# Kernel optimization log

Measured on AMD Instinct MI355X. Metric: run time of the kernel, lower is better.

Reference implementation:

```python
import jax, jax.numpy as jnp
import numpy as np

N = 50000        # nodes
E = 800000       # edges
IN, H1, H2 = 512, 256, 128
NEG_SLOPE = 0.2


def setup_inputs() -> dict:
    key = jax.random.key(0)
    k = jax.random.split(key, 6)
    X = jax.random.normal(k[0], (N, IN), jnp.float32)
    edge_index = jax.random.randint(k[1], (2, E), 0, N, dtype=jnp.int64)
    # GCNConv params: linear weight (no bias in lin) + additive bias
    W1 = jax.random.normal(k[2], (IN, H1), jnp.float32) / np.sqrt(IN).astype(np.float32)
    b1 = jnp.zeros((H1,), jnp.float32)
    W2 = jax.random.normal(k[3], (H1, H2), jnp.float32) / np.sqrt(H1).astype(np.float32)
    b2 = jnp.zeros((H2,), jnp.float32)
    return {"X": X, "edge_index": edge_index, "W1": W1, "b1": b1, "W2": W2, "b2": b2}


def gcn_conv(x, edge_index, W, b):
    """PyG GCNConv: X' = D^{-1/2} (A + I) D^{-1/2} (X W) + b."""
    src, dst = edge_index[0], edge_index[1]
    # degree with self-loops (unit edge weights)
    deg = jnp.zeros((N,), x.dtype).at[dst].add(jnp.asarray(1.0, x.dtype)) + 1.0
    dinv = jax.lax.rsqrt(deg)
    h = x @ W                                   # dense transform first (in >= out)
    coef = dinv[src] * dinv[dst]                # [E]
    msgs = h[src] * coef[:, None]               # [E, out]
    agg = jax.ops.segment_sum(msgs, dst, num_segments=N)
    agg = agg + (dinv * dinv)[:, None] * h      # self-loop contribution
    return agg + b


def reference(X, edge_index, W1, b1, W2, b2):
    Z = jax.nn.leaky_relu(gcn_conv(X, edge_index, W1, b1), NEG_SLOPE)
    Z = jax.nn.leaky_relu(gcn_conv(Z, edge_index, W2, b2), NEG_SLOPE)
    return Z
```

## Files before the change

kernel.cpp:

```cpp
#include <hip/hip_runtime.h>

constexpr int N_NODES = 50000;
constexpr int N_EDGES = 800000;
constexpr int F_IN  = 512;
constexpr int F_H1  = 256;
constexpr int F_H2  = 128;

typedef short  short8  __attribute__((ext_vector_type(8)));
typedef float  f32x4   __attribute__((ext_vector_type(4)));
typedef unsigned short us4 __attribute__((ext_vector_type(4)));

__device__ __forceinline__ unsigned short bf16_rn(float f) {
  unsigned int u = __float_as_uint(f);
  return (unsigned short)((u + 0x7FFFu + ((u >> 16) & 1u)) >> 16);
}
__device__ __forceinline__ float bf16_tof(unsigned short h) {
  return __uint_as_float(((unsigned int)h) << 16);
}


__global__ __launch_bounds__(256) void k_count(const int* __restrict__ dst,
                                               int* __restrict__ cnt, int e) {
  int i = blockIdx.x * 256 + threadIdx.x;
  if (i < e) atomicAdd(&cnt[dst[i]], 1);
}

__global__ __launch_bounds__(1024) void k_scan(const int* __restrict__ cnt,
                                               int* __restrict__ rowstart,
                                               int* __restrict__ cursor,
                                               float* __restrict__ dinv, int n) {
  __shared__ int wsum[16];
  __shared__ int carry_s;
  const int t = threadIdx.x;
  const int wid = t >> 6, lane = t & 63;
  if (t == 0) { carry_s = 0; rowstart[0] = 0; }
  __syncthreads();
  for (int base = 0; base < n; base += 4096) {
    const int i0 = base + t * 4;
    int v[4];
    if (i0 + 4 <= n) {
      const int4 v4 = *(const int4*)&cnt[i0];
      v[0] = v4.x; v[1] = v4.y; v[2] = v4.z; v[3] = v4.w;
    } else {
#pragma unroll
      for (int j = 0; j < 4; ++j) v[j] = (i0 + j < n) ? cnt[i0 + j] : 0;
    }
#pragma unroll
    for (int j = 0; j < 4; ++j)
      if (i0 + j < n) dinv[i0 + j] = rsqrtf((float)v[j] + 1.0f);
    const int tsum = v[0] + v[1] + v[2] + v[3];
    int x = tsum;
#pragma unroll
    for (int off = 1; off < 64; off <<= 1) {
      int y = __shfl_up(x, off);
      if (lane >= off) x += y;
    }
    if (lane == 63) wsum[wid] = x;
    __syncthreads();
    if (wid == 0) {
      int s = (lane < 16) ? wsum[lane] : 0;
#pragma unroll
      for (int off = 1; off < 16; off <<= 1) {
        int y = __shfl_up(s, off);
        if (lane >= off) s += y;
      }
      if (lane < 16) wsum[lane] = s;
    }
    __syncthreads();
    const int carry = carry_s;
    const int woff = (wid == 0) ? 0 : wsum[wid - 1];
    int run = carry + woff + x - tsum;
#pragma unroll
    for (int j = 0; j < 4; ++j) {
      if (i0 + j < n) {
        cursor[i0 + j] = run;
        run += v[j];
        rowstart[i0 + j + 1] = run;
      }
    }
    __syncthreads();
    if (t == 1023) carry_s = carry + woff + x;
    __syncthreads();
  }
}

__global__ __launch_bounds__(256) void k_fill(const int* __restrict__ src,
                                              const int* __restrict__ dst,
                                              int* __restrict__ cursor,
                                              const float* __restrict__ dinv,
                                              int2* __restrict__ csr, int e) {
  int i = blockIdx.x * 256 + threadIdx.x;
  if (i < e) {
    const int s = src[i], d = dst[i];
    int slot = atomicAdd(&cursor[d], 1);
    csr[slot] = make_int2(s, __float_as_int(dinv[s] * dinv[d]));
  }
}

__global__ __launch_bounds__(256) void k_wsplit2(const float* __restrict__ W1,
                                                 unsigned short* __restrict__ W1h,
                                                 unsigned short* __restrict__ W1l,
                                                 const float* __restrict__ W2,
                                                 unsigned short* __restrict__ W2h,
                                                 unsigned short* __restrict__ W2l) {
  constexpr int T1 = F_IN * F_H1;
  constexpr int T2 = F_H1 * F_H2;
  int id = blockIdx.x * 256 + threadIdx.x;
  if (id < T1) {
    int n = id / F_IN, k = id - n * F_IN;
    float f = W1[(size_t)k * F_H1 + n];
    unsigned short h = bf16_rn(f);
    W1h[id] = h;
    W1l[id] = bf16_rn(f - bf16_tof(h));
  } else if (id < T1 + T2) {
    int id2 = id - T1;
    int n = id2 / F_H1, k = id2 - n * F_H1;
    float f = W2[(size_t)k * F_H2 + n];
    unsigned short h = bf16_rn(f);
    W2h[id2] = h;
    W2l[id2] = bf16_rn(f - bf16_tof(h));
  }
}

template <bool A_IS_F32>
__global__ __launch_bounds__(512, 4) void k_mm(const float* __restrict__ Af,
                                               const unsigned short* __restrict__ Ah,
                                               const unsigned short* __restrict__ Al,
                                               const unsigned short* __restrict__ Bth,
                                               const unsigned short* __restrict__ Btl,
                                               unsigned short* __restrict__ Chh,
                                               unsigned short* __restrict__ Cll,
                                               int M, int N, int K) {
  __shared__ unsigned short Ah_s[128 * 64];
  __shared__ unsigned short Al_s[128 * 64];
  __shared__ unsigned short Bh_s[128 * 64];
  __shared__ unsigned short Bl_s[128 * 64];
  const int tid = threadIdx.x;
  const int wid = tid >> 6, lane = tid & 63;
  const int wm = wid >> 2, wn = wid & 3;
  const int lr = lane & 15, lg = lane >> 4;
  const int row0 = blockIdx.x * 128, col0 = blockIdx.y * 128;

  f32x4 acc[4][2] = {};

  float4 af0[2], af1[2];
  short8 ahr[2], alr[2];
  short8 bhr[2], blr[2];

  const int r_base = tid >> 3, g_ld = tid & 7;

  auto load_tile = [&](int k0) {
#pragma unroll
    for (int c = 0; c < 2; ++c) {
      const int r = c * 64 + r_base;
      const int gr = row0 + r;
      if (A_IS_F32) {
        af0[c] = make_float4(0.f, 0.f, 0.f, 0.f);
        af1[c] = af0[c];
        if (gr < M) {
          const float* ap = Af + (size_t)gr * K + k0 + g_ld * 8;
          af0[c] = *(const float4*)ap;
          af1[c] = *(const float4*)(ap + 4);
        }
      } else {
        ahr[c] = short8{};
        alr[c] = short8{};
        if (gr < M) {
          ahr[c] = *(const short8*)&Ah[(size_t)gr * K + k0 + g_ld * 8];
          alr[c] = *(const short8*)&Al[(size_t)gr * K + k0 + g_ld * 8];
        }
      }
      const int gcol = col0 + r;
      bhr[c] = *(const short8*)&Bth[(size_t)gcol * K + k0 + g_ld * 8];
      blr[c] = *(const short8*)&Btl[(size_t)gcol * K + k0 + g_ld * 8];
    }
  };

  auto store_tile = [&]() {
#pragma unroll
    for (int c = 0; c < 2; ++c) {
      const int r = c * 64 + r_base;
      const int gs = g_ld ^ (r & 7);
      const int doff = r * 64 + gs * 8;
      if (A_IS_F32) {
        const float fv[8] = {af0[c].x, af0[c].y, af0[c].z, af0[c].w,
                             af1[c].x, af1[c].y, af1[c].z, af1[c].w};
        unsigned short hv[8], lv[8];
#pragma unroll
        for (int j = 0; j < 8; ++j) {
          hv[j] = bf16_rn(fv[j]);
          lv[j] = bf16_rn(fv[j] - bf16_tof(hv[j]));
        }
        us4* dh = (us4*)&Ah_s[doff];
        us4* dl = (us4*)&Al_s[doff];
        dh[0] = us4{hv[0], hv[1], hv[2], hv[3]};
        dh[1] = us4{hv[4], hv[5], hv[6], hv[7]};
        dl[0] = us4{lv[0], lv[1], lv[2], lv[3]};
        dl[1] = us4{lv[4], lv[5], lv[6], lv[7]};
      } else {
        *(short8*)&Ah_s[doff] = ahr[c];
        *(short8*)&Al_s[doff] = alr[c];
      }
      *(short8*)&Bh_s[doff] = bhr[c];
      *(short8*)&Bl_s[doff] = blr[c];
    }
  };

  const int nsteps = K >> 6;
  load_tile(0);
  for (int s = 0; s < nsteps; ++s) {
    store_tile();
    __syncthreads();
    if (s + 1 < nsteps) load_tile((s + 1) << 6);
#pragma unroll
    for (int kk = 0; kk < 2; ++kk) {
      short8 ah[4], al[4], bh[2], bl[2];
#pragma unroll
      for (int m = 0; m < 4; ++m) {
        const int r = wm * 64 + m * 16 + lr;
        const int g = kk * 4 + lg;
        const int off = r * 64 + (g ^ (r & 7)) * 8;
        ah[m] = *(const short8*)&Ah_s[off];
        al[m] = *(const short8*)&Al_s[off];
      }
#pragma unroll
      for (int n = 0; n < 2; ++n) {
        const int r = wn * 32 + n * 16 + lr;
        const int g = kk * 4 + lg;
        const int off = r * 64 + (g ^ (r & 7)) * 8;
        bh[n] = *(const short8*)&Bh_s[off];
        bl[n] = *(const short8*)&Bl_s[off];
      }
#pragma unroll
      for (int m = 0; m < 4; ++m)
#pragma unroll
        for (int n = 0; n < 2; ++n)
          acc[m][n] = __builtin_amdgcn_mfma_f32_16x16x32_bf16(ah[m], bh[n],
                                                              acc[m][n], 0, 0, 0);
#pragma unroll
      for (int m = 0; m < 4; ++m)
#pragma unroll
        for (int n = 0; n < 2; ++n) {
          acc[m][n] = __builtin_amdgcn_mfma_f32_16x16x32_bf16(ah[m], bl[n],
                                                              acc[m][n], 0, 0, 0);
          acc[m][n] = __builtin_amdgcn_mfma_f32_16x16x32_bf16(al[m], bh[n],
                                                              acc[m][n], 0, 0, 0);
        }
    }
    __syncthreads();
  }
#pragma unroll
  for (int m = 0; m < 4; ++m) {
#pragma unroll
    for (int j = 0; j < 4; ++j) {
      const int row = row0 + wm * 64 + m * 16 + (lane >> 4) * 4 + j;
      if (row < M) {
        const size_t base = (size_t)row * N + col0 + wn * 32 + lr;
#pragma unroll
        for (int n = 0; n < 2; ++n) {
          const float v = acc[m][n][j];
          const unsigned short hv = bf16_rn(v);
          Chh[base + n * 16] = hv;
          Cll[base + n * 16] = bf16_rn(v - bf16_tof(hv));
        }
      }
    }
  }
}

template <int F, bool SPLIT_OUT>
__global__ __launch_bounds__(256) void k_agg(const unsigned short* __restrict__ hh,
                                             const unsigned short* __restrict__ hl,
                                             const int* __restrict__ rowstart,
                                             const int2* __restrict__ csr,
                                             const float* __restrict__ dinv,
                                             const float* __restrict__ bias,
                                             float* __restrict__ outp,
                                             unsigned short* __restrict__ outh,
                                             unsigned short* __restrict__ outl,
                                             int n) {
  constexpr int V = F / 64;
  const int node = (blockIdx.x * 256 + threadIdx.x) >> 6;
  const int lane = threadIdx.x & 63;
  if (node >= n) return;
  const float dn = dinv[node];
  const int e0 = rowstart[node];
  const int cnt = rowstart[node + 1] - e0;
  const int2* cp = csr + e0;
  float acc[V] = {};
  int i = 0;

  auto gather = [&](int s, float f[V]) {
    if constexpr (V == 4) {
      const uint2 u = *(const uint2*)(hh + (size_t)s * F + lane * 4);
      f[0] = __uint_as_float(u.x << 16);
      f[1] = __uint_as_float(u.x & 0xffff0000u);
      f[2] = __uint_as_float(u.y << 16);
      f[3] = __uint_as_float(u.y & 0xffff0000u);
    } else {
      const unsigned int u = *(const unsigned int*)(hh + (size_t)s * F + lane * 2);
      f[0] = __uint_as_float(u << 16);
      f[1] = __uint_as_float(u & 0xffff0000u);
    }
  };

  for (; i + 4 <= cnt; i += 4) {
    const int2 p0 = cp[i], p1 = cp[i + 1], p2 = cp[i + 2], p3 = cp[i + 3];
    float f0[V], f1[V], f2[V], f3[V];
    gather(p0.x, f0);
    gather(p1.x, f1);
    gather(p2.x, f2);
    gather(p3.x, f3);
    const float c0 = __int_as_float(p0.y), c1 = __int_as_float(p1.y);
    const float c2 = __int_as_float(p2.y), c3 = __int_as_float(p3.y);
#pragma unroll
    for (int j = 0; j < V; ++j)
      acc[j] += c0 * f0[j] + c1 * f1[j] + c2 * f2[j] + c3 * f3[j];
  }
  for (; i < cnt; ++i) {
    const int2 p = cp[i];
    const float c = __int_as_float(p.y);
    float f[V];
    gather(p.x, f);
#pragma unroll
    for (int j = 0; j < V; ++j) acc[j] += c * f[j];
  }

  const float sc = dn * dn;
  const unsigned short* shp = hh + (size_t)node * F + lane * V;
  const unsigned short* slp = hl + (size_t)node * F + lane * V;
  const float* bp = bias + lane * V;
  float r[V];
#pragma unroll
  for (int j = 0; j < V; ++j) {
    const float hself = bf16_tof(shp[j]) + bf16_tof(slp[j]);
    float t = acc[j] + sc * hself + bp[j];
    r[j] = fmaxf(t, 0.2f * t);
  }
  if constexpr (SPLIT_OUT) {
    unsigned short hv[V], lv[V];
#pragma unroll
    for (int j = 0; j < V; ++j) {
      hv[j] = bf16_rn(r[j]);
      lv[j] = bf16_rn(r[j] - bf16_tof(hv[j]));
    }
    if constexpr (V == 4) {
      *(us4*)&outh[(size_t)node * F + lane * 4] = us4{hv[0], hv[1], hv[2], hv[3]};
      *(us4*)&outl[(size_t)node * F + lane * 4] = us4{lv[0], lv[1], lv[2], lv[3]};
    } else {
#pragma unroll
      for (int j = 0; j < V; ++j) {
        outh[(size_t)node * F + lane * V + j] = hv[j];
        outl[(size_t)node * F + lane * V + j] = lv[j];
      }
    }
  } else {
    float* op = outp + (size_t)node * F + lane * V;
    if constexpr (V == 4) {
      *(float4*)op = make_float4(r[0], r[1], r[2], r[3]);
    } else {
      *(float2*)op = make_float2(r[0], r[1]);
    }
  }
}

extern "C" void kernel_launch(void* const* d_in, const int* in_sizes, int n_in,
                              void* d_out, int out_size, void* d_ws, size_t ws_size,
                              hipStream_t stream) {
  const float* X  = (const float*)d_in[0];
  const int*   ei = (const int*)d_in[1];
  const float* W1 = (const float*)d_in[2];
  const float* b1 = (const float*)d_in[3];
  const float* W2 = (const float*)d_in[4];
  const float* b2 = (const float*)d_in[5];
  float* out = (float*)d_out;
  const int* src = ei;
  const int* dst = ei + N_EDGES;

  char* p = (char*)d_ws;
  unsigned short* h1h = (unsigned short*)p; p += (size_t)N_NODES * F_H1 * 2;
  unsigned short* h1l = (unsigned short*)p; p += (size_t)N_NODES * F_H1 * 2;
  unsigned short* z1h = (unsigned short*)p; p += (size_t)N_NODES * F_H1 * 2;
  unsigned short* z1l = (unsigned short*)p; p += (size_t)N_NODES * F_H1 * 2;
  unsigned short* Wt1h = (unsigned short*)p; p += (size_t)F_IN * F_H1 * 2;
  unsigned short* Wt1l = (unsigned short*)p; p += (size_t)F_IN * F_H1 * 2;
  unsigned short* Wt2h = (unsigned short*)p; p += (size_t)F_H1 * F_H2 * 2;
  unsigned short* Wt2l = (unsigned short*)p; p += (size_t)F_H1 * F_H2 * 2;
  float* dinv = (float*)p;                  p += 50048 * 4;
  int* counts = (int*)p;                    p += 50048 * 4;
  int* rowstart = (int*)p;                  p += 50056 * 4;
  int* cursor = (int*)p;                    p += 50048 * 4;
  int2* csr = (int2*)p;                     p += (size_t)N_EDGES * 8;
  unsigned short* h2h = h1h;
  unsigned short* h2l = h1l;

  hipMemsetAsync(counts, 0, N_NODES * sizeof(int), stream);
  k_count<<<(N_EDGES + 255) / 256, 256, 0, stream>>>(dst, counts, N_EDGES);
  k_scan<<<1, 1024, 0, stream>>>(counts, rowstart, cursor, dinv, N_NODES);
  k_fill<<<(N_EDGES + 255) / 256, 256, 0, stream>>>(src, dst, cursor, dinv, csr,
                                                    N_EDGES);

  k_wsplit2<<<(F_IN * F_H1 + F_H1 * F_H2 + 255) / 256, 256, 0, stream>>>(
      W1, Wt1h, Wt1l, W2, Wt2h, Wt2l);

  dim3 g1((N_NODES + 127) / 128, F_H1 / 128);
  k_mm<true><<<g1, 512, 0, stream>>>(X, nullptr, nullptr, Wt1h, Wt1l, h1h, h1l,
                                     N_NODES, F_H1, F_IN);
  k_agg<F_H1, true><<<(N_NODES + 3) / 4, 256, 0, stream>>>(
      h1h, h1l, rowstart, csr, dinv, b1, nullptr, z1h, z1l, N_NODES);

  dim3 g2((N_NODES + 127) / 128, F_H2 / 128);
  k_mm<false><<<g2, 512, 0, stream>>>(nullptr, z1h, z1l, Wt2h, Wt2l, h2h, h2l,
                                      N_NODES, F_H2, F_H1);
  k_agg<F_H2, false><<<(N_NODES + 3) / 4, 256, 0, stream>>>(
      h2h, h2l, rowstart, csr, dinv, b2, out, nullptr, nullptr, N_NODES);
}
```

Baseline: 332.9 us.

## Double-buffer LDS in split-bf16 GEMM with 32-wide k-steps and prefetch

Restructures the GEMM main loop to use two LDS buffers of 32-wide k slices, with register prefetch two steps ahead, so global loads, LDS writes and MFMA compute overlap and only one barrier is needed per step. The LDS layout changes to a k-group-major arrangement without the XOR swizzle, and the f32 to hi/lo bf16 split now truncates instead of rounding. It also raises wave priority around the MFMA blocks. Risks include LDS bank conflicts from the unswizzled layout, higher register pressure, and slightly different numerics from truncation.

```diff
diff --git a/kernel.cpp b/kernel.cpp
--- a/kernel.cpp
+++ b/kernel.cpp
@@ -131,124 +131,120 @@
                                                unsigned short* __restrict__ Chh,
                                                unsigned short* __restrict__ Cll,
                                                int M, int N, int K) {
-  __shared__ unsigned short Ah_s[128 * 64];
-  __shared__ unsigned short Al_s[128 * 64];
-  __shared__ unsigned short Bh_s[128 * 64];
-  __shared__ unsigned short Bl_s[128 * 64];
+  __shared__ unsigned short lds[2 * 16384];
   const int tid = threadIdx.x;
   const int wid = tid >> 6, lane = tid & 63;
   const int wm = wid >> 2, wn = wid & 3;
   const int lr = lane & 15, lg = lane >> 4;
   const int row0 = blockIdx.x * 128, col0 = blockIdx.y * 128;
 
+  const int sg = wid & 3;
+  const int sr = ((wid >> 2) << 6) + lane;
+  const int s_off = sg * 1024 + sr * 8;
+  const bool a_ok = (row0 + sr) < M;
+  const size_t a_row = (size_t)(row0 + sr) * K;
+  const size_t b_row = (size_t)(col0 + sr) * K;
+
   f32x4 acc[4][2] = {};
 
-  float4 af0[2], af1[2];
-  short8 ahr[2], alr[2];
-  short8 bhr[2], blr[2];
-
-  const int r_base = tid >> 3, g_ld = tid & 7;
-
-  auto load_tile = [&](int k0) {
-#pragma unroll
-    for (int c = 0; c < 2; ++c) {
-      const int r = c * 64 + r_base;
-      const int gr = row0 + r;
-      if (A_IS_F32) {
-        af0[c] = make_float4(0.f, 0.f, 0.f, 0.f);
-        af1[c] = af0[c];
-        if (gr < M) {
-          const float* ap = Af + (size_t)gr * K + k0 + g_ld * 8;
-          af0[c] = *(const float4*)ap;
-          af1[c] = *(const float4*)(ap + 4);
-        }
-      } else {
-        ahr[c] = short8{};
-        alr[c] = short8{};
-        if (gr < M) {
-          ahr[c] = *(const short8*)&Ah[(size_t)gr * K + k0 + g_ld * 8];
-          alr[c] = *(const short8*)&Al[(size_t)gr * K + k0 + g_ld * 8];
-        }
-      }
-      const int gcol = col0 + r;
-      bhr[c] = *(const short8*)&Bth[(size_t)gcol * K + k0 + g_ld * 8];
-      blr[c] = *(const short8*)&Btl[(size_t)gcol * K + k0 + g_ld * 8];
-    }
-  };
-
-  auto store_tile = [&]() {
-#pragma unroll
-    for (int c = 0; c < 2; ++c) {
-      const int r = c * 64 + r_base;
-      const int gs = g_ld ^ (r & 7);
-      const int doff = r * 64 + gs * 8;
-      if (A_IS_F32) {
-        const float fv[8] = {af0[c].x, af0[c].y, af0[c].z, af0[c].w,
-                             af1[c].x, af1[c].y, af1[c].z, af1[c].w};
-        unsigned short hv[8], lv[8];
-#pragma unroll
-        for (int j = 0; j < 8; ++j) {
-          hv[j] = bf16_rn(fv[j]);
-          lv[j] = bf16_rn(fv[j] - bf16_tof(hv[j]));
-        }
-        us4* dh = (us4*)&Ah_s[doff];
-        us4* dl = (us4*)&Al_s[doff];
-        dh[0] = us4{hv[0], hv[1], hv[2], hv[3]};
-        dh[1] = us4{hv[4], hv[5], hv[6], hv[7]};
-        dl[0] = us4{lv[0], lv[1], lv[2], lv[3]};
-        dl[1] = us4{lv[4], lv[5], lv[6], lv[7]};
-      } else {
-        *(short8*)&Ah_s[doff] = ahr[c];
-        *(short8*)&Al_s[doff] = alr[c];
-      }
-      *(short8*)&Bh_s[doff] = bhr[c];
-      *(short8*)&Bl_s[doff] = blr[c];
-    }
-  };
-
-  const int nsteps = K >> 6;
-  load_tile(0);
-  for (int s = 0; s < nsteps; ++s) {
-    store_tile();
-    __syncthreads();
-    if (s + 1 < nsteps) load_tile((s + 1) << 6);
-#pragma unroll
-    for (int kk = 0; kk < 2; ++kk) {
-      short8 ah[4], al[4], bh[2], bl[2];
-#pragma unroll
-      for (int m = 0; m < 4; ++m) {
-        const int r = wm * 64 + m * 16 + lr;
-        const int g = kk * 4 + lg;
-        const int off = r * 64 + (g ^ (r & 7)) * 8;
-        ah[m] = *(const short8*)&Ah_s[off];
-        al[m] = *(const short8*)&Al_s[off];
-      }
-#pragma unroll
-      for (int n = 0; n < 2; ++n) {
-        const int r = wn * 32 + n * 16 + lr;
-        const int g = kk * 4 + lg;
-        const int off = r * 64 + (g ^ (r & 7)) * 8;
-        bh[n] = *(const short8*)&Bh_s[off];
-        bl[n] = *(const short8*)&Bl_s[off];
-      }
-#pragma unroll
-      for (int m = 0; m < 4; ++m)
-#pragma unroll
-        for (int n = 0; n < 2; ++n)
-          acc[m][n] = __builtin_amdgcn_mfma_f32_16x16x32_bf16(ah[m], bh[n],
-                                                              acc[m][n], 0, 0, 0);
-#pragma unroll
-      for (int m = 0; m < 4; ++m)
-#pragma unroll
-        for (int n = 0; n < 2; ++n) {
-          acc[m][n] = __builtin_amdgcn_mfma_f32_16x16x32_bf16(ah[m], bl[n],
-                                                              acc[m][n], 0, 0, 0);
-          acc[m][n] = __builtin_amdgcn_mfma_f32_16x16x32_bf16(al[m], bh[n],
-                                                              acc[m][n], 0, 0, 0);
-        }
-    }
-    __syncthreads();
-  }
+  float4 a0A, a1A, a0B, a1B;
+  short8 ahA, alA, ahB, alB;
+  short8 bhA, blA, bhB, blB;
+
+#define LOADSET(SUF, k0)                                                      \
+  {                                                                           \
+    const int kk_ = (k0) + sg * 8;                                            \
+    if (A_IS_F32) {                                                           \
+      a0##SUF = make_float4(0.f, 0.f, 0.f, 0.f);                              \
+      a1##SUF = a0##SUF;                                                      \
+      if (a_ok) {                                                             \
+        const float* ap = Af + a_row + kk_;                                   \
+        a0##SUF = *(const float4*)ap;                                         \
+        a1##SUF = *(const float4*)(ap + 4);                                   \
+      }                                                                       \
+    } else {                                                                  \
+      ah##SUF = short8{};                                                     \
+      al##SUF = short8{};                                                     \
+      if (a_ok) {                                                             \
+        ah##SUF = *(const short8*)&Ah[a_row + kk_];                           \
+        al##SUF = *(const short8*)&Al[a_row + kk_];                           \
+      }                                                                       \
+    }                                                                         \
+    bh##SUF = *(const short8*)&Bth[b_row + kk_];                              \
+    bl##SUF = *(const short8*)&Btl[b_row + kk_];                              \
+  }
+
+#define WRITESET(SUF, buf)                                                    \
+  {                                                                           \
+    unsigned short* base = &lds[(buf)*16384 + s_off];                         \
+    if (A_IS_F32) {                                                           \
+      const float fv[8] = {a0##SUF.x, a0##SUF.y, a0##SUF.z, a0##SUF.w,        \
+                           a1##SUF.x, a1##SUF.y, a1##SUF.z, a1##SUF.w};       \
+      short8 hv, lv;                                                          \
+      _Pragma("unroll") for (int j_ = 0; j_ < 8; ++j_) {                      \
+        const unsigned int u_ = __float_as_uint(fv[j_]);                      \
+        hv[j_] = (short)(u_ >> 16);                                           \
+        const float lo_ = fv[j_] - __uint_as_float(u_ & 0xffff0000u);         \
+        lv[j_] = (short)(__float_as_uint(lo_) >> 16);                         \
+      }                                                                       \
+      *(short8*)&base[0] = hv;                                                \
+      *(short8*)&base[4096] = lv;                                             \
+    } else {                                                                  \
+      *(short8*)&base[0] = ah##SUF;                                           \
+      *(short8*)&base[4096] = al##SUF;                                        \
+    }                                                                         \
+    *(short8*)&base[8192] = bh##SUF;                                          \
+    *(short8*)&base[12288] = bl##SUF;                                         \
+  }
+
+#define COMPUTE(buf)                                                          \
+  {                                                                           \
+    short8 fah[4], fal[4], fbh[2], fbl[2];                                    \
+    const unsigned short* lb = &lds[(buf)*16384 + lg * 1024];                 \
+    _Pragma("unroll") for (int m_ = 0; m_ < 4; ++m_) {                        \
+      const int off_ = (wm * 64 + m_ * 16 + lr) * 8;                          \
+      fah[m_] = *(const short8*)&lb[off_];                                    \
+      fal[m_] = *(const short8*)&lb[4096 + off_];                             \
+    }                                                                         \
+    _Pragma("unroll") for (int n_ = 0; n_ < 2; ++n_) {                        \
+      const int off_ = (wn * 32 + n_ * 16 + lr) * 8;                          \
+      fbh[n_] = *(const short8*)&lb[8192 + off_];                             \
+      fbl[n_] = *(const short8*)&lb[12288 + off_];                            \
+    }                                                                         \
+    __builtin_amdgcn_s_setprio(1);                                            \
+    _Pragma("unroll") for (int m_ = 0; m_ < 4; ++m_)                          \
+      _Pragma("unroll") for (int n_ = 0; n_ < 2; ++n_)                        \
+        acc[m_][n_] = __builtin_amdgcn_mfma_f32_16x16x32_bf16(                \
+            fah[m_], fbh[n_], acc[m_][n_], 0, 0, 0);                          \
+    _Pragma("unroll") for (int m_ = 0; m_ < 4; ++m_)                          \
+      _Pragma("unroll") for (int n_ = 0; n_ < 2; ++n_) {                      \
+        acc[m_][n_] = __builtin_amdgcn_mfma_f32_16x16x32_bf16(                \
+            fah[m_], fbl[n_], acc[m_][n_], 0, 0, 0);                          \
+        acc[m_][n_] = __builtin_amdgcn_mfma_f32_16x16x32_bf16(                \
+            fal[m_], fbh[n_], acc[m_][n_], 0, 0, 0);                          \
+      }                                                                       \
+    __builtin_amdgcn_s_setprio(0);                                            \
+  }
+
+  const int S = K >> 5;
+  LOADSET(B, 0)
+  WRITESET(B, 0)
+  LOADSET(A, 32)
+  LOADSET(B, 64)
+  for (int h = 0; h < S; h += 2) {
+    __syncthreads();
+    WRITESET(A, 1)
+    if (h + 3 < S) LOADSET(A, (h + 3) * 32)
+    COMPUTE(0)
+    __syncthreads();
+    if (h + 2 < S) WRITESET(B, 0)
+    if (h + 4 < S) LOADSET(B, (h + 4) * 32)
+    COMPUTE(1)
+  }
+#undef LOADSET
+#undef WRITESET
+#undef COMPUTE
+
 #pragma unroll
   for (int m = 0; m < 4; ++m) {
 #pragma unroll
```

New measurement: 414.4 us. 24.5% more time.
